# Kernel optimization log

Hardware: AMD Instinct MI355X
Metric: run time of the kernel (lower is better)

## Reference

```python
import jax, jax.numpy as jnp
import numpy as np

B, T, C = 128, 512, 128  # batch, seq_len, num_tags


def setup_inputs() -> dict:
    key = jax.random.key(0)
    k1, k2, k3 = jax.random.split(key, 3)
    labels = jax.random.randint(k1, (B, T), 0, C)
    y_true = jax.nn.one_hot(labels, C, dtype=jnp.float32)  # dense one-hot targets
    y_pred = jax.random.normal(k2, (B, T, C), dtype=jnp.float32)  # emission scores
    mask = jnp.ones((B, T), dtype=jnp.float32)
    # glorot_uniform for (C,C): limit = sqrt(6/(C+C))
    limit = np.sqrt(6.0 / (C + C)).astype(np.float32)
    trans = jax.random.uniform(k3, (C, C), dtype=jnp.float32, minval=-limit, maxval=limit)
    return {"y_true": y_true, "y_pred": y_pred, "mask": mask, "trans": trans}


def reference(y_true, y_pred, mask, trans):
    # Faithful translation of ConditionalRandomField.dense_loss (lr_multiplier=1).
    m = mask[..., None]                      # (B,T,1)
    y_true = y_true * m
    y_pred = y_pred * m
    # real path score
    emission = jnp.einsum('bnc,bnc->b', y_true, y_pred)
    transition = jnp.einsum('bni,ij,bnj->b', y_true[:, :-1], trans, y_true[:, 1:])
    real_path_score = emission + transition  # (B,)
    # forward algorithm: sequential logsumexp recurrence (K.rnn equivalent)
    init = y_pred[:, 0]                      # (B,C)
    xs = (jnp.swapaxes(y_pred[:, 1:], 0, 1),  # (T-1,B,C)
          jnp.swapaxes(mask[:, 1:], 0, 1))    # (T-1,B)

    def step(state, xm):
        x_t, m_t = xm
        # state: (B,C) alpha; trans: (C,C)
        new = jax.nn.logsumexp(state[:, :, None] + trans[None, :, :], axis=1) + x_t
        state = jnp.where(m_t[:, None] > 0, new, state)  # masked steps carry prev state
        return state, None

    last, _ = jax.lax.scan(step, init, xs)
    all_paths_score = jax.nn.logsumexp(last, axis=1)  # (B,)
    return all_paths_score - real_path_score          # (B,) per-sample CRF NLL
```

## Files before the change

### kernel.cpp

```cpp
#include <hip/hip_runtime.h>

#define BB 128
#define TT 512
#define CC 128

typedef short short8 __attribute__((ext_vector_type(8)));
typedef float f32x4  __attribute__((ext_vector_type(4)));
typedef unsigned u32x4 __attribute__((ext_vector_type(4)));
typedef unsigned u32x2 __attribute__((ext_vector_type(2)));

__device__ __forceinline__ unsigned pk_trunc(float a, float b) {
    return __builtin_amdgcn_perm(__float_as_uint(a), __float_as_uint(b), 0x03020706u);
}
__device__ __forceinline__ unsigned short f2bf(float f) {
    unsigned u = __float_as_uint(f);
    u += 0x7fffu + ((u >> 16) & 1u);
    return (unsigned short)(u >> 16);
}
__device__ __forceinline__ float lo16f(unsigned u) { return __uint_as_float(u << 16); }
__device__ __forceinline__ float hi16f(unsigned u) { return __uint_as_float(u & 0xffff0000u); }

#define MFMA16(A, B, C) __builtin_amdgcn_mfma_f32_16x16x32_bf16((A), (B), (C), 0, 0, 0)

__global__ __launch_bounds__(256, 1) void crf_all(
    const float* __restrict__ y_true, const float* __restrict__ y_pred,
    const float* __restrict__ mask, const float* __restrict__ trans,
    float* __restrict__ out)
{
    __shared__ __align__(16) unsigned sbuf[2][1024];
    __shared__ float red[4][16];

    const int tid  = threadIdx.x;
    const int lane = tid & 63;
    const int w    = tid >> 6;
    const int bq   = lane & 15;
    const int q    = lane >> 4;

    if (blockIdx.x >= 8) {
        const int rb  = blockIdx.x - 8;
        const int ts  = w * 128;
        const int te  = min(ts + 128, TT - 1);
        const float* yt_b = y_true + (size_t)rb * TT * CC;
        const float* yp_b = y_pred + (size_t)rb * TT * CC;
        const float* m_b  = mask + (size_t)rb * TT;

        float em = 0.f, tr = 0.f;
        int lprev = 0; float mprev = 0.f;
        const float* ytr = yt_b + ts * CC;
        const float* ypr = yp_b + ts * CC;
        float cyt0 = ytr[lane], cyt1 = ytr[lane + 64];
        float cyp0 = ypr[lane], cyp1 = ypr[lane + 64];
        float cm = m_b[ts];
        for (int t = ts; t <= te; ++t) {
            float nyt0 = 0.f, nyt1 = 0.f, nyp0 = 0.f, nyp1 = 0.f, nm = 0.f;
            if (t < te) {
                const float* ytn = yt_b + (t + 1) * CC;
                const float* ypn = yp_b + (t + 1) * CC;
                nyt0 = ytn[lane]; nyt1 = ytn[lane + 64];
                nyp0 = ypn[lane]; nyp1 = ypn[lane + 64];
                nm = m_b[t + 1];
            }
            unsigned long long b0 = __ballot(cyt0 > 0.5f);
            unsigned long long b1 = __ballot(cyt1 > 0.5f);
            int l = b0 ? (__ffsll(b0) - 1) : (64 + __ffsll(b1) - 1);
            float v0 = __shfl(cyp0, l & 63);
            float v1 = __shfl(cyp1, l & 63);
            float v  = (l < 64) ? v0 : v1;
            if (lane == 0) {
                if (t < ts + 128) em += cm * cm * v;
                if (t > ts)       tr += mprev * cm * trans[lprev * CC + l];
            }
            lprev = l; mprev = cm;
            cyt0 = nyt0; cyt1 = nyt1; cyp0 = nyp0; cyp1 = nyp1; cm = nm;
        }
        if (lane == 0) atomicAdd(&out[rb], -(em + tr));
        return;
    }

    const int g = blockIdx.x;
    const float* yb   = y_pred + (size_t)(g * 16 + bq) * TT * CC;
    const float* mrow = mask + (size_t)(g * 16 + bq) * TT;
    const int ch0 = 32 * w + 4 * q;

    const float4 i0 = *(const float4*)(yb + ch0);
    const float4 i1 = *(const float4*)(yb + ch0 + 16);
    const float  m0 = mrow[0];
    float4 pfa[4], pfb[4]; float pfm[4];
    #pragma unroll
    for (int p = 0; p < 4; ++p) {
        pfa[p] = *(const float4*)(yb + (size_t)(1 + p) * CC + ch0);
        pfb[p] = *(const float4*)(yb + (size_t)(1 + p) * CC + ch0 + 16);
        pfm[p] = mrow[1 + p];
    }

    short8 Af[2][4];
    #pragma unroll
    for (int n2 = 0; n2 < 2; ++n2) {
        const int j = (2 * w + n2) * 16 + bq;
        #pragma unroll
        for (int kt = 0; kt < 4; ++kt) {
            #pragma unroll
            for (int e = 0; e < 8; ++e)
                Af[n2][kt][e] = (short)f2bf(__expf(trans[(kt * 32 + q * 8 + e) * CC + j]));
        }
    }

    const int swz = (bq & 7) << 2;
    const int rw0 = bq * 64 + (( 0 + 4 * q) ^ swz);
    const int rw1 = bq * 64 + ((16 + 4 * q) ^ swz);
    const int rw2 = bq * 64 + ((32 + 4 * q) ^ swz);
    const int rw3 = bq * 64 + ((48 + 4 * q) ^ swz);
    const int ww0 = bq * 64 + ((16 * w + 2 * q) ^ swz);
    const int ww1 = bq * 64 + ((16 * w + 8 + 2 * q) ^ swz);

    {
        unsigned p0 = pk_trunc(__expf(i0.x * m0), __expf(i0.y * m0));
        unsigned p1 = pk_trunc(__expf(i0.z * m0), __expf(i0.w * m0));
        unsigned p2 = pk_trunc(__expf(i1.x * m0), __expf(i1.y * m0));
        unsigned p3 = pk_trunc(__expf(i1.z * m0), __expf(i1.w * m0));
        u32x2 a; a[0] = p0; a[1] = p1;
        u32x2 b; b[0] = p2; b[1] = p3;
        *(u32x2*)(&sbuf[0][0] + ww0) = a;
        *(u32x2*)(&sbuf[0][0] + ww1) = b;
    }
    asm volatile("s_waitcnt lgkmcnt(0)" ::: "memory");
    __builtin_amdgcn_s_barrier();
    asm volatile("" ::: "memory");

    float lacc = 0.f;

    auto dostep = [&](const int p, const int rpar, const bool ap, const int tn) {
        const unsigned* sb = &sbuf[rpar][0];
        unsigned* sw = &sbuf[rpar ^ 1][0];
        u32x4 B0 = *(const u32x4*)(sb + rw0);
        u32x4 B1 = *(const u32x4*)(sb + rw1);
        u32x4 B2 = *(const u32x4*)(sb + rw2);
        u32x4 B3 = *(const u32x4*)(sb + rw3);
        float pend = 1.f;
        if (ap) {
            float bc = __shfl(lo16f(B0[0]), bq, 64);
            pend = __builtin_amdgcn_rcpf(bc);
            lacc += __logf(bc);
        }
        union { u32x4 u; short8 s; } c0, c1, c2, c3;
        c0.u = B0; c1.u = B1; c2.u = B2; c3.u = B3;
        f32x4 a0 = {0.f, 0.f, 0.f, 0.f}, a1 = {0.f, 0.f, 0.f, 0.f};
        a0 = MFMA16(Af[0][0], c0.s, a0); a0 = MFMA16(Af[0][1], c1.s, a0);
        a0 = MFMA16(Af[0][2], c2.s, a0); a0 = MFMA16(Af[0][3], c3.s, a0);
        a1 = MFMA16(Af[1][0], c0.s, a1); a1 = MFMA16(Af[1][1], c1.s, a1);
        a1 = MFMA16(Af[1][2], c2.s, a1); a1 = MFMA16(Af[1][3], c3.s, a1);
        const float mm = pfm[p];
        const float4 va = pfa[p], vb = pfb[p];
        float e0 = __expf(va.x * mm), e1 = __expf(va.y * mm);
        float e2 = __expf(va.z * mm), e3 = __expf(va.w * mm);
        float f0 = __expf(vb.x * mm), f1 = __expf(vb.y * mm);
        float f2 = __expf(vb.z * mm), f3 = __expf(vb.w * mm);
        float v0 = a0[0] * e0, v1 = a0[1] * e1, v2 = a0[2] * e2, v3 = a0[3] * e3;
        float u0 = a1[0] * f0, u1 = a1[1] * f1, u2 = a1[2] * f2, u3 = a1[3] * f3;
        if (ap) {
            v0 *= pend; v1 *= pend; v2 *= pend; v3 *= pend;
            u0 *= pend; u1 *= pend; u2 *= pend; u3 *= pend;
        }
        unsigned n0 = pk_trunc(v0, v1), n1 = pk_trunc(v2, v3);
        unsigned n2 = pk_trunc(u0, u1), n3 = pk_trunc(u2, u3);
        if (__ballot(mm <= 0.f)) {
            u32x2 o0 = *(const u32x2*)(sb + ww0);
            u32x2 o1 = *(const u32x2*)(sb + ww1);
            unsigned k0 = pk_trunc(lo16f(o0[0]) * pend, hi16f(o0[0]) * pend);
            unsigned k1 = pk_trunc(lo16f(o0[1]) * pend, hi16f(o0[1]) * pend);
            unsigned k2 = pk_trunc(lo16f(o1[0]) * pend, hi16f(o1[0]) * pend);
            unsigned k3 = pk_trunc(lo16f(o1[1]) * pend, hi16f(o1[1]) * pend);
            const bool kk = (mm <= 0.f);
            n0 = kk ? k0 : n0; n1 = kk ? k1 : n1;
            n2 = kk ? k2 : n2; n3 = kk ? k3 : n3;
        }
        u32x2 wv0; wv0[0] = n0; wv0[1] = n1;
        u32x2 wv1; wv1[0] = n2; wv1[1] = n3;
        *(u32x2*)(sw + ww0) = wv0;
        *(u32x2*)(sw + ww1) = wv1;
        if (tn >= 0) {
            pfa[p] = *(const float4*)(yb + (size_t)tn * CC + ch0);
            pfb[p] = *(const float4*)(yb + (size_t)tn * CC + ch0 + 16);
            pfm[p] = mrow[tn];
        }
        asm volatile("s_waitcnt lgkmcnt(0)" ::: "memory");
        __builtin_amdgcn_s_barrier();
        asm volatile("" ::: "memory");
    };

    for (int tt = 1; tt <= 505; tt += 4) {
        int t4 = tt + 4, t5 = tt + 5, t6 = tt + 6, t7 = tt + 7;
        if (t7 > TT - 1) t7 = TT - 1;
        dostep(0, 0, true,  t4);
        dostep(1, 1, false, t5);
        dostep(2, 0, false, t6);
        dostep(3, 1, false, t7);
    }
    dostep(0, 0, true,  -1);
    dostep(1, 1, false, -1);

    {
        const unsigned* sb = &sbuf[0][0];
        u32x4 B0 = *(const u32x4*)(sb + rw0);
        u32x4 B1 = *(const u32x4*)(sb + rw1);
        u32x4 B2 = *(const u32x4*)(sb + rw2);
        u32x4 B3 = *(const u32x4*)(sb + rw3);
        union { u32x4 u; short8 s; } c0, c1, c2, c3;
        c0.u = B0; c1.u = B1; c2.u = B2; c3.u = B3;
        f32x4 a0 = {0.f, 0.f, 0.f, 0.f}, a1 = {0.f, 0.f, 0.f, 0.f};
        a0 = MFMA16(Af[0][0], c0.s, a0); a0 = MFMA16(Af[0][1], c1.s, a0);
        a0 = MFMA16(Af[0][2], c2.s, a0); a0 = MFMA16(Af[0][3], c3.s, a0);
        a1 = MFMA16(Af[1][0], c0.s, a1); a1 = MFMA16(Af[1][1], c1.s, a1);
        a1 = MFMA16(Af[1][2], c2.s, a1); a1 = MFMA16(Af[1][3], c3.s, a1);
        const float mm = pfm[2];
        const float4 va = pfa[2], vb = pfb[2];
        float e0 = __expf(va.x * mm), e1 = __expf(va.y * mm);
        float e2 = __expf(va.z * mm), e3 = __expf(va.w * mm);
        float f0 = __expf(vb.x * mm), f1 = __expf(vb.y * mm);
        float f2 = __expf(vb.z * mm), f3 = __expf(vb.w * mm);
        float ssum = a0[0] * e0 + a0[1] * e1 + a0[2] * e2 + a0[3] * e3
                   + a1[0] * f0 + a1[1] * f1 + a1[2] * f2 + a1[3] * f3;
        if (__ballot(mm <= 0.f)) {
            u32x2 o0 = *(const u32x2*)(sb + ww0);
            u32x2 o1 = *(const u32x2*)(sb + ww1);
            float os = lo16f(o0[0]) + hi16f(o0[0]) + lo16f(o0[1]) + hi16f(o0[1])
                     + lo16f(o1[0]) + hi16f(o1[0]) + lo16f(o1[1]) + hi16f(o1[1]);
            ssum = (mm <= 0.f) ? os : ssum;
        }
        ssum += __shfl_xor(ssum, 16, 64);
        ssum += __shfl_xor(ssum, 32, 64);
        if (lane < 16) red[w][lane] = ssum;
        asm volatile("s_waitcnt lgkmcnt(0)" ::: "memory");
        __builtin_amdgcn_s_barrier();
        asm volatile("" ::: "memory");
        if (w == 0 && lane < 16) {
            float tot = red[0][lane] + red[1][lane] + red[2][lane] + red[3][lane];
            atomicAdd(&out[g * 16 + lane], __logf(tot) + lacc);
        }
    }
}

extern "C" void kernel_launch(void* const* d_in, const int* in_sizes, int n_in,
                              void* d_out, int out_size, void* d_ws, size_t ws_size,
                              hipStream_t stream) {
    (void)in_sizes; (void)n_in; (void)out_size; (void)d_ws; (void)ws_size;
    const float* y_true = (const float*)d_in[0];
    const float* y_pred = (const float*)d_in[1];
    const float* mask   = (const float*)d_in[2];
    const float* trans  = (const float*)d_in[3];
    float* out = (float*)d_out;

    hipMemsetAsync(out, 0, BB * sizeof(float), stream);
    crf_all<<<dim3(8 + BB), 256, 0, stream>>>(y_true, y_pred, mask, trans, out);
}
```

Baseline: 255.7 us.

## Pack two batch groups per 512-thread block in forward recurrence

Doubles the block size to 512 threads so each forward-algorithm block handles two independent 16-sample groups, with separate LDS buffers and reductions per half. Grid shrinks from 8+128 to 4+128 blocks, and the real-path blocks split the sequence into 64-step chunks over 8 waves. The two groups now share every block-wide barrier, so each step's sync has to wait for both groups. The intent is better latency hiding from having more waves per CU on the serial recurrence.

```diff
diff --git a/kernel.cpp b/kernel.cpp
--- a/kernel.cpp
+++ b/kernel.cpp
@@ -22,13 +22,13 @@
 
 #define MFMA16(A, B, C) __builtin_amdgcn_mfma_f32_16x16x32_bf16((A), (B), (C), 0, 0, 0)
 
-__global__ __launch_bounds__(256, 1) void crf_all(
+__global__ __launch_bounds__(512, 1) void crf_all(
     const float* __restrict__ y_true, const float* __restrict__ y_pred,
     const float* __restrict__ mask, const float* __restrict__ trans,
     float* __restrict__ out)
 {
-    __shared__ __align__(16) unsigned sbuf[2][1024];
-    __shared__ float red[4][16];
+    __shared__ __align__(16) unsigned sbuf[2][2][1024];
+    __shared__ float red[2][4][16];
 
     const int tid  = threadIdx.x;
     const int lane = tid & 63;
@@ -36,10 +36,10 @@
     const int bq   = lane & 15;
     const int q    = lane >> 4;
 
-    if (blockIdx.x >= 8) {
-        const int rb  = blockIdx.x - 8;
-        const int ts  = w * 128;
-        const int te  = min(ts + 128, TT - 1);
+    if (blockIdx.x >= 4) {
+        const int rb  = blockIdx.x - 4;
+        const int ts  = w * 64;
+        const int te  = min(ts + 64, TT - 1);
         const float* yt_b = y_true + (size_t)rb * TT * CC;
         const float* yp_b = y_pred + (size_t)rb * TT * CC;
         const float* m_b  = mask + (size_t)rb * TT;
@@ -67,8 +67,8 @@
             float v1 = __shfl(cyp1, l & 63);
             float v  = (l < 64) ? v0 : v1;
             if (lane == 0) {
-                if (t < ts + 128) em += cm * cm * v;
-                if (t > ts)       tr += mprev * cm * trans[lprev * CC + l];
+                if (t < ts + 64) em += cm * cm * v;
+                if (t > ts)      tr += mprev * cm * trans[lprev * CC + l];
             }
             lprev = l; mprev = cm;
             cyt0 = nyt0; cyt1 = nyt1; cyp0 = nyp0; cyp1 = nyp1; cm = nm;
@@ -77,10 +77,12 @@
         return;
     }
 
-    const int g = blockIdx.x;
+    const int h  = w >> 2;
+    const int wv = w & 3;
+    const int g  = blockIdx.x * 2 + h;
     const float* yb   = y_pred + (size_t)(g * 16 + bq) * TT * CC;
     const float* mrow = mask + (size_t)(g * 16 + bq) * TT;
-    const int ch0 = 32 * w + 4 * q;
+    const int ch0 = 32 * wv + 4 * q;
 
     const float4 i0 = *(const float4*)(yb + ch0);
     const float4 i1 = *(const float4*)(yb + ch0 + 16);
@@ -96,7 +98,7 @@
     short8 Af[2][4];
     #pragma unroll
     for (int n2 = 0; n2 < 2; ++n2) {
-        const int j = (2 * w + n2) * 16 + bq;
+        const int j = (2 * wv + n2) * 16 + bq;
         #pragma unroll
         for (int kt = 0; kt < 4; ++kt) {
             #pragma unroll
@@ -110,8 +112,8 @@
     const int rw1 = bq * 64 + ((16 + 4 * q) ^ swz);
     const int rw2 = bq * 64 + ((32 + 4 * q) ^ swz);
     const int rw3 = bq * 64 + ((48 + 4 * q) ^ swz);
-    const int ww0 = bq * 64 + ((16 * w + 2 * q) ^ swz);
-    const int ww1 = bq * 64 + ((16 * w + 8 + 2 * q) ^ swz);
+    const int ww0 = bq * 64 + ((16 * wv + 2 * q) ^ swz);
+    const int ww1 = bq * 64 + ((16 * wv + 8 + 2 * q) ^ swz);
 
     {
         unsigned p0 = pk_trunc(__expf(i0.x * m0), __expf(i0.y * m0));
@@ -120,8 +122,8 @@
         unsigned p3 = pk_trunc(__expf(i1.z * m0), __expf(i1.w * m0));
         u32x2 a; a[0] = p0; a[1] = p1;
         u32x2 b; b[0] = p2; b[1] = p3;
-        *(u32x2*)(&sbuf[0][0] + ww0) = a;
-        *(u32x2*)(&sbuf[0][0] + ww1) = b;
+        *(u32x2*)(&sbuf[h][0][0] + ww0) = a;
+        *(u32x2*)(&sbuf[h][0][0] + ww1) = b;
     }
     asm volatile("s_waitcnt lgkmcnt(0)" ::: "memory");
     __builtin_amdgcn_s_barrier();
@@ -130,8 +132,8 @@
     float lacc = 0.f;
 
     auto dostep = [&](const int p, const int rpar, const bool ap, const int tn) {
-        const unsigned* sb = &sbuf[rpar][0];
-        unsigned* sw = &sbuf[rpar ^ 1][0];
+        const unsigned* sb = &sbuf[h][rpar][0];
+        unsigned* sw = &sbuf[h][rpar ^ 1][0];
         u32x4 B0 = *(const u32x4*)(sb + rw0);
         u32x4 B1 = *(const u32x4*)(sb + rw1);
         u32x4 B2 = *(const u32x4*)(sb + rw2);
@@ -200,7 +202,7 @@
     dostep(1, 1, false, -1);
 
     {
-        const unsigned* sb = &sbuf[0][0];
+        const unsigned* sb = &sbuf[h][0][0];
         u32x4 B0 = *(const u32x4*)(sb + rw0);
         u32x4 B1 = *(const u32x4*)(sb + rw1);
         u32x4 B2 = *(const u32x4*)(sb + rw2);
@@ -229,12 +231,13 @@
         }
         ssum += __shfl_xor(ssum, 16, 64);
         ssum += __shfl_xor(ssum, 32, 64);
-        if (lane < 16) red[w][lane] = ssum;
+        if (lane < 16) red[h][wv][lane] = ssum;
         asm volatile("s_waitcnt lgkmcnt(0)" ::: "memory");
         __builtin_amdgcn_s_barrier();
         asm volatile("" ::: "memory");
-        if (w == 0 && lane < 16) {
-            float tot = red[0][lane] + red[1][lane] + red[2][lane] + red[3][lane];
+        if (wv == 0 && lane < 16) {
+            float tot = red[h][0][lane] + red[h][1][lane]
+                      + red[h][2][lane] + red[h][3][lane];
             atomicAdd(&out[g * 16 + lane], __logf(tot) + lacc);
         }
     }
@@ -251,5 +254,5 @@
     float* out = (float*)d_out;
 
     hipMemsetAsync(out, 0, BB * sizeof(float), stream);
-    crf_all<<<dim3(8 + BB), 256, 0, stream>>>(y_true, y_pred, mask, trans, out);
-}
+    crf_all<<<dim3(4 + BB), 512, 0, stream>>>(y_true, y_pred, mask, trans, out);
+}
```

Result: slower. 419.2 us (+64.0%).

## Split scan and real-path into separate kernels, use two waves per scan block

Applied to the files above, without the earlier changes.

The forward-recurrence scan now runs in its own kernel with 128 threads (two waves) per block, each wave owning 64 output tags and issuing four MFMA tiles per k-step. This halves the number of waves taking part in each per-step barrier. The real-path score moves to a separate kernel launched afterwards on the same stream. The cost is twice the MFMA and exp work per wave, more registers, and an extra launch that may no longer overlap with the scan.

```diff
diff --git a/kernel.cpp b/kernel.cpp
--- a/kernel.cpp
+++ b/kernel.cpp
@@ -22,13 +22,12 @@
 
 #define MFMA16(A, B, C) __builtin_amdgcn_mfma_f32_16x16x32_bf16((A), (B), (C), 0, 0, 0)
 
-__global__ __launch_bounds__(256, 1) void crf_all(
-    const float* __restrict__ y_true, const float* __restrict__ y_pred,
-    const float* __restrict__ mask, const float* __restrict__ trans,
-    float* __restrict__ out)
+__global__ __launch_bounds__(128, 1) void crf_scan(
+    const float* __restrict__ y_pred, const float* __restrict__ mask,
+    const float* __restrict__ trans, float* __restrict__ out)
 {
     __shared__ __align__(16) unsigned sbuf[2][1024];
-    __shared__ float red[4][16];
+    __shared__ float red[2][16];
 
     const int tid  = threadIdx.x;
     const int lane = tid & 63;
@@ -36,72 +35,33 @@
     const int bq   = lane & 15;
     const int q    = lane >> 4;
 
-    if (blockIdx.x >= 8) {
-        const int rb  = blockIdx.x - 8;
-        const int ts  = w * 128;
-        const int te  = min(ts + 128, TT - 1);
-        const float* yt_b = y_true + (size_t)rb * TT * CC;
-        const float* yp_b = y_pred + (size_t)rb * TT * CC;
-        const float* m_b  = mask + (size_t)rb * TT;
-
-        float em = 0.f, tr = 0.f;
-        int lprev = 0; float mprev = 0.f;
-        const float* ytr = yt_b + ts * CC;
-        const float* ypr = yp_b + ts * CC;
-        float cyt0 = ytr[lane], cyt1 = ytr[lane + 64];
-        float cyp0 = ypr[lane], cyp1 = ypr[lane + 64];
-        float cm = m_b[ts];
-        for (int t = ts; t <= te; ++t) {
-            float nyt0 = 0.f, nyt1 = 0.f, nyp0 = 0.f, nyp1 = 0.f, nm = 0.f;
-            if (t < te) {
-                const float* ytn = yt_b + (t + 1) * CC;
-                const float* ypn = yp_b + (t + 1) * CC;
-                nyt0 = ytn[lane]; nyt1 = ytn[lane + 64];
-                nyp0 = ypn[lane]; nyp1 = ypn[lane + 64];
-                nm = m_b[t + 1];
-            }
-            unsigned long long b0 = __ballot(cyt0 > 0.5f);
-            unsigned long long b1 = __ballot(cyt1 > 0.5f);
-            int l = b0 ? (__ffsll(b0) - 1) : (64 + __ffsll(b1) - 1);
-            float v0 = __shfl(cyp0, l & 63);
-            float v1 = __shfl(cyp1, l & 63);
-            float v  = (l < 64) ? v0 : v1;
-            if (lane == 0) {
-                if (t < ts + 128) em += cm * cm * v;
-                if (t > ts)       tr += mprev * cm * trans[lprev * CC + l];
-            }
-            lprev = l; mprev = cm;
-            cyt0 = nyt0; cyt1 = nyt1; cyp0 = nyp0; cyp1 = nyp1; cm = nm;
-        }
-        if (lane == 0) atomicAdd(&out[rb], -(em + tr));
-        return;
-    }
-
     const int g = blockIdx.x;
     const float* yb   = y_pred + (size_t)(g * 16 + bq) * TT * CC;
     const float* mrow = mask + (size_t)(g * 16 + bq) * TT;
-    const int ch0 = 32 * w + 4 * q;
-
-    const float4 i0 = *(const float4*)(yb + ch0);
-    const float4 i1 = *(const float4*)(yb + ch0 + 16);
-    const float  m0 = mrow[0];
-    float4 pfa[4], pfb[4]; float pfm[4];
+    const int ch0 = 64 * w + 4 * q;
+
+    float4 i4[4];
+    #pragma unroll
+    for (int c = 0; c < 4; ++c) i4[c] = *(const float4*)(yb + ch0 + 16 * c);
+    const float m0 = mrow[0];
+    float4 pf[4][4]; float pfm[4];
     #pragma unroll
     for (int p = 0; p < 4; ++p) {
-        pfa[p] = *(const float4*)(yb + (size_t)(1 + p) * CC + ch0);
-        pfb[p] = *(const float4*)(yb + (size_t)(1 + p) * CC + ch0 + 16);
+        #pragma unroll
+        for (int c = 0; c < 4; ++c)
+            pf[p][c] = *(const float4*)(yb + (size_t)(1 + p) * CC + ch0 + 16 * c);
         pfm[p] = mrow[1 + p];
     }
 
-    short8 Af[2][4];
-    #pragma unroll
-    for (int n2 = 0; n2 < 2; ++n2) {
-        const int j = (2 * w + n2) * 16 + bq;
+    short8 Af[4][4];
+    #pragma unroll
+    for (int nt = 0; nt < 4; ++nt) {
+        const int j = (4 * w + nt) * 16 + bq;
         #pragma unroll
         for (int kt = 0; kt < 4; ++kt) {
             #pragma unroll
             for (int e = 0; e < 8; ++e)
-                Af[n2][kt][e] = (short)f2bf(__expf(trans[(kt * 32 + q * 8 + e) * CC + j]));
+                Af[nt][kt][e] = (short)f2bf(__expf(trans[(kt * 32 + q * 8 + e) * CC + j]));
         }
     }
 
@@ -110,18 +70,17 @@
     const int rw1 = bq * 64 + ((16 + 4 * q) ^ swz);
     const int rw2 = bq * 64 + ((32 + 4 * q) ^ swz);
     const int rw3 = bq * 64 + ((48 + 4 * q) ^ swz);
-    const int ww0 = bq * 64 + ((16 * w + 2 * q) ^ swz);
-    const int ww1 = bq * 64 + ((16 * w + 8 + 2 * q) ^ swz);
-
-    {
-        unsigned p0 = pk_trunc(__expf(i0.x * m0), __expf(i0.y * m0));
-        unsigned p1 = pk_trunc(__expf(i0.z * m0), __expf(i0.w * m0));
-        unsigned p2 = pk_trunc(__expf(i1.x * m0), __expf(i1.y * m0));
-        unsigned p3 = pk_trunc(__expf(i1.z * m0), __expf(i1.w * m0));
+    int ww[4];
+    #pragma unroll
+    for (int nt = 0; nt < 4; ++nt)
+        ww[nt] = bq * 64 + ((32 * w + 8 * nt + 2 * q) ^ swz);
+
+    #pragma unroll
+    for (int c = 0; c < 4; ++c) {
+        unsigned p0 = pk_trunc(__expf(i4[c].x * m0), __expf(i4[c].y * m0));
+        unsigned p1 = pk_trunc(__expf(i4[c].z * m0), __expf(i4[c].w * m0));
         u32x2 a; a[0] = p0; a[1] = p1;
-        u32x2 b; b[0] = p2; b[1] = p3;
-        *(u32x2*)(&sbuf[0][0] + ww0) = a;
-        *(u32x2*)(&sbuf[0][0] + ww1) = b;
+        *(u32x2*)(&sbuf[0][0] + ww[c]) = a;
     }
     asm volatile("s_waitcnt lgkmcnt(0)" ::: "memory");
     __builtin_amdgcn_s_barrier();
@@ -136,6 +95,13 @@
         u32x4 B1 = *(const u32x4*)(sb + rw1);
         u32x4 B2 = *(const u32x4*)(sb + rw2);
         u32x4 B3 = *(const u32x4*)(sb + rw3);
+        const float mm = pfm[p];
+        float e[4][4];
+        #pragma unroll
+        for (int c = 0; c < 4; ++c) {
+            e[c][0] = __expf(pf[p][c].x * mm); e[c][1] = __expf(pf[p][c].y * mm);
+            e[c][2] = __expf(pf[p][c].z * mm); e[c][3] = __expf(pf[p][c].w * mm);
+        }
         float pend = 1.f;
         if (ap) {
             float bc = __shfl(lo16f(B0[0]), bq, 64);
@@ -144,43 +110,46 @@
         }
         union { u32x4 u; short8 s; } c0, c1, c2, c3;
         c0.u = B0; c1.u = B1; c2.u = B2; c3.u = B3;
-        f32x4 a0 = {0.f, 0.f, 0.f, 0.f}, a1 = {0.f, 0.f, 0.f, 0.f};
-        a0 = MFMA16(Af[0][0], c0.s, a0); a0 = MFMA16(Af[0][1], c1.s, a0);
-        a0 = MFMA16(Af[0][2], c2.s, a0); a0 = MFMA16(Af[0][3], c3.s, a0);
-        a1 = MFMA16(Af[1][0], c0.s, a1); a1 = MFMA16(Af[1][1], c1.s, a1);
-        a1 = MFMA16(Af[1][2], c2.s, a1); a1 = MFMA16(Af[1][3], c3.s, a1);
-        const float mm = pfm[p];
-        const float4 va = pfa[p], vb = pfb[p];
-        float e0 = __expf(va.x * mm), e1 = __expf(va.y * mm);
-        float e2 = __expf(va.z * mm), e3 = __expf(va.w * mm);
-        float f0 = __expf(vb.x * mm), f1 = __expf(vb.y * mm);
-        float f2 = __expf(vb.z * mm), f3 = __expf(vb.w * mm);
-        float v0 = a0[0] * e0, v1 = a0[1] * e1, v2 = a0[2] * e2, v3 = a0[3] * e3;
-        float u0 = a1[0] * f0, u1 = a1[1] * f1, u2 = a1[2] * f2, u3 = a1[3] * f3;
-        if (ap) {
-            v0 *= pend; v1 *= pend; v2 *= pend; v3 *= pend;
-            u0 *= pend; u1 *= pend; u2 *= pend; u3 *= pend;
-        }
-        unsigned n0 = pk_trunc(v0, v1), n1 = pk_trunc(v2, v3);
-        unsigned n2 = pk_trunc(u0, u1), n3 = pk_trunc(u2, u3);
+        f32x4 acc[4];
+        #pragma unroll
+        for (int nt = 0; nt < 4; ++nt) { f32x4 z = {0.f,0.f,0.f,0.f}; acc[nt] = z; }
+        #pragma unroll
+        for (int nt = 0; nt < 4; ++nt) acc[nt] = MFMA16(Af[nt][0], c0.s, acc[nt]);
+        #pragma unroll
+        for (int nt = 0; nt < 4; ++nt) acc[nt] = MFMA16(Af[nt][1], c1.s, acc[nt]);
+        #pragma unroll
+        for (int nt = 0; nt < 4; ++nt) acc[nt] = MFMA16(Af[nt][2], c2.s, acc[nt]);
+        #pragma unroll
+        for (int nt = 0; nt < 4; ++nt) acc[nt] = MFMA16(Af[nt][3], c3.s, acc[nt]);
+        unsigned nn[4][2];
+        #pragma unroll
+        for (int nt = 0; nt < 4; ++nt) {
+            float v0 = acc[nt][0] * e[nt][0], v1 = acc[nt][1] * e[nt][1];
+            float v2 = acc[nt][2] * e[nt][2], v3 = acc[nt][3] * e[nt][3];
+            if (ap) { v0 *= pend; v1 *= pend; v2 *= pend; v3 *= pend; }
+            nn[nt][0] = pk_trunc(v0, v1);
+            nn[nt][1] = pk_trunc(v2, v3);
+        }
         if (__ballot(mm <= 0.f)) {
-            u32x2 o0 = *(const u32x2*)(sb + ww0);
-            u32x2 o1 = *(const u32x2*)(sb + ww1);
-            unsigned k0 = pk_trunc(lo16f(o0[0]) * pend, hi16f(o0[0]) * pend);
-            unsigned k1 = pk_trunc(lo16f(o0[1]) * pend, hi16f(o0[1]) * pend);
-            unsigned k2 = pk_trunc(lo16f(o1[0]) * pend, hi16f(o1[0]) * pend);
-            unsigned k3 = pk_trunc(lo16f(o1[1]) * pend, hi16f(o1[1]) * pend);
-            const bool kk = (mm <= 0.f);
-            n0 = kk ? k0 : n0; n1 = kk ? k1 : n1;
-            n2 = kk ? k2 : n2; n3 = kk ? k3 : n3;
-        }
-        u32x2 wv0; wv0[0] = n0; wv0[1] = n1;
-        u32x2 wv1; wv1[0] = n2; wv1[1] = n3;
-        *(u32x2*)(sw + ww0) = wv0;
-        *(u32x2*)(sw + ww1) = wv1;
+            #pragma unroll
+            for (int nt = 0; nt < 4; ++nt) {
+                u32x2 o = *(const u32x2*)(sb + ww[nt]);
+                unsigned k0 = pk_trunc(lo16f(o[0]) * pend, hi16f(o[0]) * pend);
+                unsigned k1 = pk_trunc(lo16f(o[1]) * pend, hi16f(o[1]) * pend);
+                const bool kk = (mm <= 0.f);
+                nn[nt][0] = kk ? k0 : nn[nt][0];
+                nn[nt][1] = kk ? k1 : nn[nt][1];
+            }
+        }
+        #pragma unroll
+        for (int nt = 0; nt < 4; ++nt) {
+            u32x2 wv2; wv2[0] = nn[nt][0]; wv2[1] = nn[nt][1];
+            *(u32x2*)(sw + ww[nt]) = wv2;
+        }
         if (tn >= 0) {
-            pfa[p] = *(const float4*)(yb + (size_t)tn * CC + ch0);
-            pfb[p] = *(const float4*)(yb + (size_t)tn * CC + ch0 + 16);
+            #pragma unroll
+            for (int c = 0; c < 4; ++c)
+                pf[p][c] = *(const float4*)(yb + (size_t)tn * CC + ch0 + 16 * c);
             pfm[p] = mrow[tn];
         }
         asm volatile("s_waitcnt lgkmcnt(0)" ::: "memory");
@@ -205,26 +174,38 @@
         u32x4 B1 = *(const u32x4*)(sb + rw1);
         u32x4 B2 = *(const u32x4*)(sb + rw2);
         u32x4 B3 = *(const u32x4*)(sb + rw3);
+        const float mm = pfm[2];
+        float e[4][4];
+        #pragma unroll
+        for (int c = 0; c < 4; ++c) {
+            e[c][0] = __expf(pf[2][c].x * mm); e[c][1] = __expf(pf[2][c].y * mm);
+            e[c][2] = __expf(pf[2][c].z * mm); e[c][3] = __expf(pf[2][c].w * mm);
+        }
         union { u32x4 u; short8 s; } c0, c1, c2, c3;
         c0.u = B0; c1.u = B1; c2.u = B2; c3.u = B3;
-        f32x4 a0 = {0.f, 0.f, 0.f, 0.f}, a1 = {0.f, 0.f, 0.f, 0.f};
-        a0 = MFMA16(Af[0][0], c0.s, a0); a0 = MFMA16(Af[0][1], c1.s, a0);
-        a0 = MFMA16(Af[0][2], c2.s, a0); a0 = MFMA16(Af[0][3], c3.s, a0);
-        a1 = MFMA16(Af[1][0], c0.s, a1); a1 = MFMA16(Af[1][1], c1.s, a1);
-        a1 = MFMA16(Af[1][2], c2.s, a1); a1 = MFMA16(Af[1][3], c3.s, a1);
-        const float mm = pfm[2];
-        const float4 va = pfa[2], vb = pfb[2];
-        float e0 = __expf(va.x * mm), e1 = __expf(va.y * mm);
-        float e2 = __expf(va.z * mm), e3 = __expf(va.w * mm);
-        float f0 = __expf(vb.x * mm), f1 = __expf(vb.y * mm);
-        float f2 = __expf(vb.z * mm), f3 = __expf(vb.w * mm);
-        float ssum = a0[0] * e0 + a0[1] * e1 + a0[2] * e2 + a0[3] * e3
-                   + a1[0] * f0 + a1[1] * f1 + a1[2] * f2 + a1[3] * f3;
+        f32x4 acc[4];
+        #pragma unroll
+        for (int nt = 0; nt < 4; ++nt) { f32x4 z = {0.f,0.f,0.f,0.f}; acc[nt] = z; }
+        #pragma unroll
+        for (int nt = 0; nt < 4; ++nt) acc[nt] = MFMA16(Af[nt][0], c0.s, acc[nt]);
+        #pragma unroll
+        for (int nt = 0; nt < 4; ++nt) acc[nt] = MFMA16(Af[nt][1], c1.s, acc[nt]);
+        #pragma unroll
+        for (int nt = 0; nt < 4; ++nt) acc[nt] = MFMA16(Af[nt][2], c2.s, acc[nt]);
+        #pragma unroll
+        for (int nt = 0; nt < 4; ++nt) acc[nt] = MFMA16(Af[nt][3], c3.s, acc[nt]);
+        float ssum = 0.f;
+        #pragma unroll
+        for (int nt = 0; nt < 4; ++nt)
+            ssum += acc[nt][0] * e[nt][0] + acc[nt][1] * e[nt][1]
+                  + acc[nt][2] * e[nt][2] + acc[nt][3] * e[nt][3];
         if (__ballot(mm <= 0.f)) {
-            u32x2 o0 = *(const u32x2*)(sb + ww0);
-            u32x2 o1 = *(const u32x2*)(sb + ww1);
-            float os = lo16f(o0[0]) + hi16f(o0[0]) + lo16f(o0[1]) + hi16f(o0[1])
-                     + lo16f(o1[0]) + hi16f(o1[0]) + lo16f(o1[1]) + hi16f(o1[1]);
+            float os = 0.f;
+            #pragma unroll
+            for (int nt = 0; nt < 4; ++nt) {
+                u32x2 o = *(const u32x2*)(sb + ww[nt]);
+                os += lo16f(o[0]) + hi16f(o[0]) + lo16f(o[1]) + hi16f(o[1]);
+            }
             ssum = (mm <= 0.f) ? os : ssum;
         }
         ssum += __shfl_xor(ssum, 16, 64);
@@ -234,10 +215,57 @@
         __builtin_amdgcn_s_barrier();
         asm volatile("" ::: "memory");
         if (w == 0 && lane < 16) {
-            float tot = red[0][lane] + red[1][lane] + red[2][lane] + red[3][lane];
+            float tot = red[0][lane] + red[1][lane];
             atomicAdd(&out[g * 16 + lane], __logf(tot) + lacc);
         }
     }
+}
+
+__global__ __launch_bounds__(256, 1) void crf_real(
+    const float* __restrict__ y_true, const float* __restrict__ y_pred,
+    const float* __restrict__ mask, const float* __restrict__ trans,
+    float* __restrict__ out)
+{
+    const int tid  = threadIdx.x;
+    const int lane = tid & 63;
+    const int w    = tid >> 6;
+    const int rb   = blockIdx.x;
+    const int ts   = w * 128;
+    const int te   = min(ts + 128, TT - 1);
+    const float* yt_b = y_true + (size_t)rb * TT * CC;
+    const float* yp_b = y_pred + (size_t)rb * TT * CC;
+    const float* m_b  = mask + (size_t)rb * TT;
+
+    float em = 0.f, tr = 0.f;
+    int lprev = 0; float mprev = 0.f;
+    const float* ytr = yt_b + ts * CC;
+    const float* ypr = yp_b + ts * CC;
+    float cyt0 = ytr[lane], cyt1 = ytr[lane + 64];
+    float cyp0 = ypr[lane], cyp1 = ypr[lane + 64];
+    float cm = m_b[ts];
+    for (int t = ts; t <= te; ++t) {
+        float nyt0 = 0.f, nyt1 = 0.f, nyp0 = 0.f, nyp1 = 0.f, nm = 0.f;
+        if (t < te) {
+            const float* ytn = yt_b + (t + 1) * CC;
+            const float* ypn = yp_b + (t + 1) * CC;
+            nyt0 = ytn[lane]; nyt1 = ytn[lane + 64];
+            nyp0 = ypn[lane]; nyp1 = ypn[lane + 64];
+            nm = m_b[t + 1];
+        }
+        unsigned long long b0 = __ballot(cyt0 > 0.5f);
+        unsigned long long b1 = __ballot(cyt1 > 0.5f);
+        int l = b0 ? (__ffsll(b0) - 1) : (64 + __ffsll(b1) - 1);
+        float v0 = __shfl(cyp0, l & 63);
+        float v1 = __shfl(cyp1, l & 63);
+        float v  = (l < 64) ? v0 : v1;
+        if (lane == 0) {
+            if (t < ts + 128) em += cm * cm * v;
+            if (t > ts)       tr += mprev * cm * trans[lprev * CC + l];
+        }
+        lprev = l; mprev = cm;
+        cyt0 = nyt0; cyt1 = nyt1; cyp0 = nyp0; cyp1 = nyp1; cm = nm;
+    }
+    if (lane == 0) atomicAdd(&out[rb], -(em + tr));
 }
 
 extern "C" void kernel_launch(void* const* d_in, const int* in_sizes, int n_in,
@@ -251,5 +279,6 @@
     float* out = (float*)d_out;
 
     hipMemsetAsync(out, 0, BB * sizeof(float), stream);
-    crf_all<<<dim3(8 + BB), 256, 0, stream>>>(y_true, y_pred, mask, trans, out);
-}
+    crf_scan<<<dim3(8), 128, 0, stream>>>(y_pred, mask, trans, out);
+    crf_real<<<dim3(BB), 256, 0, stream>>>(y_true, y_pred, mask, trans, out);
+}
```

Result: slower. 352.2 us (+37.7%).

## Keep own-wave state slice in registers via shuffles, reorder K-tiles per wave

Applied to the files above, without the earlier changes.

Each wave now builds the MFMA B-operand for its own 32-channel K-slice directly from the values it just produced, using cross-lane shuffles, instead of reading them back from LDS. It rotates the K-tile order per wave so the register-held slice goes first and can issue before the LDS reads of the other three slices land. The MFMA chain is split into two independent accumulators to shorten the dependency chain, and the normaliser is read straight from LDS instead of through a shuffle. This aims to cut LDS read latency and serial MFMA dependency in the per-timestep critical path, at the cost of extra shuffle instructions and registers.

```diff
diff --git a/kernel.cpp b/kernel.cpp
--- a/kernel.cpp
+++ b/kernel.cpp
@@ -21,6 +21,86 @@
 __device__ __forceinline__ float hi16f(unsigned u) { return __uint_as_float(u & 0xffff0000u); }
 
 #define MFMA16(A, B, C) __builtin_amdgcn_mfma_f32_16x16x32_bf16((A), (B), (C), 0, 0, 0)
+
+#define BUILD_BFO(n00, n01, n10, n11) do {                                     \
+    const int sA_ = bq + 16 * ((2 * q) & 3);                                   \
+    const int sB_ = bq + 16 * ((2 * q + 1) & 3);                               \
+    unsigned a00 = __shfl((n00), sA_, 64), a10 = __shfl((n10), sA_, 64);       \
+    unsigned a01 = __shfl((n01), sA_, 64), a11 = __shfl((n11), sA_, 64);       \
+    unsigned b00 = __shfl((n00), sB_, 64), b10 = __shfl((n10), sB_, 64);       \
+    unsigned b01 = __shfl((n01), sB_, 64), b11 = __shfl((n11), sB_, 64);       \
+    const bool hi_ = (q >> 1) != 0;                                            \
+    BfO[0] = hi_ ? a10 : a00;                                                  \
+    BfO[1] = hi_ ? a11 : a01;                                                  \
+    BfO[2] = hi_ ? b10 : b00;                                                  \
+    BfO[3] = hi_ ? b11 : b01;                                                  \
+} while (0)
+
+#define DOSTEP(AP_, P_, RPAR_, TN_) do {                                       \
+    const unsigned* sb = &sbuf[RPAR_][0];                                      \
+    unsigned* sw = &sbuf[(RPAR_) ^ 1][0];                                      \
+    u32x4 Rv1 = *(const u32x4*)(sb + rd1);                                     \
+    u32x4 Rv2 = *(const u32x4*)(sb + rd2);                                     \
+    u32x4 Rv3 = *(const u32x4*)(sb + rd3);                                     \
+    unsigned bcu = 0;                                                          \
+    if (AP_) bcu = sb[bcaddr];                    \
+    const float mm = pfm[P_];                                                  \
+    float e0[4], e1[4];                                                        \
+    e0[0] = __expf(pfa[P_].x * mm); e0[1] = __expf(pfa[P_].y * mm);            \
+    e0[2] = __expf(pfa[P_].z * mm); e0[3] = __expf(pfa[P_].w * mm);            \
+    e1[0] = __expf(pfb[P_].x * mm); e1[1] = __expf(pfb[P_].y * mm);            \
+    e1[2] = __expf(pfb[P_].z * mm); e1[3] = __expf(pfb[P_].w * mm);            \
+    union { u32x4 u; short8 s; } cO, c1, c2, c3;                               \
+    cO.u[0] = BfO[0]; cO.u[1] = BfO[1]; cO.u[2] = BfO[2]; cO.u[3] = BfO[3];    \
+    c1.u = Rv1; c2.u = Rv2; c3.u = Rv3;                                        \
+    f32x4 aA0 = {0.f,0.f,0.f,0.f}, aA1 = {0.f,0.f,0.f,0.f};                    \
+    f32x4 aB0 = {0.f,0.f,0.f,0.f}, aB1 = {0.f,0.f,0.f,0.f};                    \
+    aA0 = MFMA16(AfP[0][0], cO.s, aA0);  aA1 = MFMA16(AfP[1][0], cO.s, aA1);   \
+    aA0 = MFMA16(AfP[0][1], c1.s, aA0);  aA1 = MFMA16(AfP[1][1], c1.s, aA1);   \
+    aB0 = MFMA16(AfP[0][2], c2.s, aB0);  aB1 = MFMA16(AfP[1][2], c2.s, aB1);   \
+    aB0 = MFMA16(AfP[0][3], c3.s, aB0);  aB1 = MFMA16(AfP[1][3], c3.s, aB1);   \
+    f32x4 ac0 = aA0 + aB0, ac1 = aA1 + aB1;                                    \
+    float pend = 1.f;                                                          \
+    if (AP_) {                                                                 \
+        float bc = lo16f(bcu);                                                 \
+        pend = __builtin_amdgcn_rcpf(bc);                                      \
+        lacc += __logf(bc);                                                    \
+    }                                                                          \
+    float v00 = ac0[0]*e0[0], v01 = ac0[1]*e0[1];                              \
+    float v02 = ac0[2]*e0[2], v03 = ac0[3]*e0[3];                              \
+    float v10 = ac1[0]*e1[0], v11 = ac1[1]*e1[1];                              \
+    float v12 = ac1[2]*e1[2], v13 = ac1[3]*e1[3];                              \
+    if (AP_) {                                                                 \
+        v00 *= pend; v01 *= pend; v02 *= pend; v03 *= pend;                    \
+        v10 *= pend; v11 *= pend; v12 *= pend; v13 *= pend;                    \
+    }                                                                          \
+    unsigned n00 = pk_trunc(v00, v01), n01 = pk_trunc(v02, v03);               \
+    unsigned n10 = pk_trunc(v10, v11), n11 = pk_trunc(v12, v13);               \
+    if (__ballot(mm <= 0.f)) {                  \
+        u32x2 o0 = *(const u32x2*)(sb + wwA);                                  \
+        u32x2 o1 = *(const u32x2*)(sb + wwB);                                  \
+        unsigned k00 = pk_trunc(lo16f(o0[0]) * pend, hi16f(o0[0]) * pend);     \
+        unsigned k01 = pk_trunc(lo16f(o0[1]) * pend, hi16f(o0[1]) * pend);     \
+        unsigned k10 = pk_trunc(lo16f(o1[0]) * pend, hi16f(o1[0]) * pend);     \
+        unsigned k11 = pk_trunc(lo16f(o1[1]) * pend, hi16f(o1[1]) * pend);     \
+        const bool kk = (mm <= 0.f);                                           \
+        n00 = kk ? k00 : n00; n01 = kk ? k01 : n01;                            \
+        n10 = kk ? k10 : n10; n11 = kk ? k11 : n11;                            \
+    }                                                                          \
+    u32x2 wv0; wv0[0] = n00; wv0[1] = n01;                                     \
+    u32x2 wv1; wv1[0] = n10; wv1[1] = n11;                                     \
+    *(u32x2*)(sw + wwA) = wv0;                                                 \
+    *(u32x2*)(sw + wwB) = wv1;                                                 \
+    BUILD_BFO(n00, n01, n10, n11);                \
+    if ((TN_) >= 0) {                                  \
+        pfa[P_] = *(const float4*)(yb + (size_t)(TN_) * CC + ch0);             \
+        pfb[P_] = *(const float4*)(yb + (size_t)(TN_) * CC + ch0 + 16);        \
+        pfm[P_] = mrow[TN_];                                                   \
+    }                                                                          \
+    asm volatile("s_waitcnt lgkmcnt(0)" ::: "memory");                         \
+    __builtin_amdgcn_s_barrier();                 \
+    asm volatile("" ::: "memory");                                             \
+} while (0)
 
 __global__ __launch_bounds__(256, 1) void crf_all(
     const float* __restrict__ y_true, const float* __restrict__ y_pred,
@@ -33,8 +113,6 @@
     const int tid  = threadIdx.x;
     const int lane = tid & 63;
     const int w    = tid >> 6;
-    const int bq   = lane & 15;
-    const int q    = lane >> 4;
 
     if (blockIdx.x >= 8) {
         const int rb  = blockIdx.x - 8;
@@ -77,7 +155,9 @@
         return;
     }
 
-    const int g = blockIdx.x;
+    const int bq = lane & 15;
+    const int q  = lane >> 4;
+    const int g  = blockIdx.x;
     const float* yb   = y_pred + (size_t)(g * 16 + bq) * TT * CC;
     const float* mrow = mask + (size_t)(g * 16 + bq) * TT;
     const int ch0 = 32 * w + 4 * q;
@@ -93,35 +173,39 @@
         pfm[p] = mrow[1 + p];
     }
 
-    short8 Af[2][4];
+    short8 AfP[2][4];
     #pragma unroll
     for (int n2 = 0; n2 < 2; ++n2) {
         const int j = (2 * w + n2) * 16 + bq;
         #pragma unroll
-        for (int kt = 0; kt < 4; ++kt) {
+        for (int i = 0; i < 4; ++i) {
+            const int kt = (w + i) & 3;
             #pragma unroll
             for (int e = 0; e < 8; ++e)
-                Af[n2][kt][e] = (short)f2bf(__expf(trans[(kt * 32 + q * 8 + e) * CC + j]));
+                AfP[n2][i][e] = (short)f2bf(__expf(trans[(kt * 32 + q * 8 + e) * CC + j]));
         }
     }
 
     const int swz = (bq & 7) << 2;
-    const int rw0 = bq * 64 + (( 0 + 4 * q) ^ swz);
-    const int rw1 = bq * 64 + ((16 + 4 * q) ^ swz);
-    const int rw2 = bq * 64 + ((32 + 4 * q) ^ swz);
-    const int rw3 = bq * 64 + ((48 + 4 * q) ^ swz);
-    const int ww0 = bq * 64 + ((16 * w + 2 * q) ^ swz);
-    const int ww1 = bq * 64 + ((16 * w + 8 + 2 * q) ^ swz);
+    const int rd1 = bq * 64 + ((((w + 1) & 3) * 16 + 4 * q) ^ swz);
+    const int rd2 = bq * 64 + ((((w + 2) & 3) * 16 + 4 * q) ^ swz);
+    const int rd3 = bq * 64 + ((((w + 3) & 3) * 16 + 4 * q) ^ swz);
+    const int wwA = bq * 64 + ((16 * w + 2 * q) ^ swz);
+    const int wwB = bq * 64 + ((16 * w + 8 + 2 * q) ^ swz);
+    const int bcaddr = bq * 64 + swz;
+
+    unsigned BfO[4];
 
     {
-        unsigned p0 = pk_trunc(__expf(i0.x * m0), __expf(i0.y * m0));
-        unsigned p1 = pk_trunc(__expf(i0.z * m0), __expf(i0.w * m0));
-        unsigned p2 = pk_trunc(__expf(i1.x * m0), __expf(i1.y * m0));
-        unsigned p3 = pk_trunc(__expf(i1.z * m0), __expf(i1.w * m0));
-        u32x2 a; a[0] = p0; a[1] = p1;
-        u32x2 b; b[0] = p2; b[1] = p3;
-        *(u32x2*)(&sbuf[0][0] + ww0) = a;
-        *(u32x2*)(&sbuf[0][0] + ww1) = b;
+        unsigned n00 = pk_trunc(__expf(i0.x * m0), __expf(i0.y * m0));
+        unsigned n01 = pk_trunc(__expf(i0.z * m0), __expf(i0.w * m0));
+        unsigned n10 = pk_trunc(__expf(i1.x * m0), __expf(i1.y * m0));
+        unsigned n11 = pk_trunc(__expf(i1.z * m0), __expf(i1.w * m0));
+        u32x2 a; a[0] = n00; a[1] = n01;
+        u32x2 b; b[0] = n10; b[1] = n11;
+        *(u32x2*)(&sbuf[0][0] + wwA) = a;
+        *(u32x2*)(&sbuf[0][0] + wwB) = b;
+        BUILD_BFO(n00, n01, n10, n11);
     }
     asm volatile("s_waitcnt lgkmcnt(0)" ::: "memory");
     __builtin_amdgcn_s_barrier();
@@ -129,100 +213,43 @@
 
     float lacc = 0.f;
 
-    auto dostep = [&](const int p, const int rpar, const bool ap, const int tn) {
-        const unsigned* sb = &sbuf[rpar][0];
-        unsigned* sw = &sbuf[rpar ^ 1][0];
-        u32x4 B0 = *(const u32x4*)(sb + rw0);
-        u32x4 B1 = *(const u32x4*)(sb + rw1);
-        u32x4 B2 = *(const u32x4*)(sb + rw2);
-        u32x4 B3 = *(const u32x4*)(sb + rw3);
-        float pend = 1.f;
-        if (ap) {
-            float bc = __shfl(lo16f(B0[0]), bq, 64);
-            pend = __builtin_amdgcn_rcpf(bc);
-            lacc += __logf(bc);
-        }
-        union { u32x4 u; short8 s; } c0, c1, c2, c3;
-        c0.u = B0; c1.u = B1; c2.u = B2; c3.u = B3;
-        f32x4 a0 = {0.f, 0.f, 0.f, 0.f}, a1 = {0.f, 0.f, 0.f, 0.f};
-        a0 = MFMA16(Af[0][0], c0.s, a0); a0 = MFMA16(Af[0][1], c1.s, a0);
-        a0 = MFMA16(Af[0][2], c2.s, a0); a0 = MFMA16(Af[0][3], c3.s, a0);
-        a1 = MFMA16(Af[1][0], c0.s, a1); a1 = MFMA16(Af[1][1], c1.s, a1);
-        a1 = MFMA16(Af[1][2], c2.s, a1); a1 = MFMA16(Af[1][3], c3.s, a1);
-        const float mm = pfm[p];
-        const float4 va = pfa[p], vb = pfb[p];
-        float e0 = __expf(va.x * mm), e1 = __expf(va.y * mm);
-        float e2 = __expf(va.z * mm), e3 = __expf(va.w * mm);
-        float f0 = __expf(vb.x * mm), f1 = __expf(vb.y * mm);
-        float f2 = __expf(vb.z * mm), f3 = __expf(vb.w * mm);
-        float v0 = a0[0] * e0, v1 = a0[1] * e1, v2 = a0[2] * e2, v3 = a0[3] * e3;
-        float u0 = a1[0] * f0, u1 = a1[1] * f1, u2 = a1[2] * f2, u3 = a1[3] * f3;
-        if (ap) {
-            v0 *= pend; v1 *= pend; v2 *= pend; v3 *= pend;
-            u0 *= pend; u1 *= pend; u2 *= pend; u3 *= pend;
-        }
-        unsigned n0 = pk_trunc(v0, v1), n1 = pk_trunc(v2, v3);
-        unsigned n2 = pk_trunc(u0, u1), n3 = pk_trunc(u2, u3);
-        if (__ballot(mm <= 0.f)) {
-            u32x2 o0 = *(const u32x2*)(sb + ww0);
-            u32x2 o1 = *(const u32x2*)(sb + ww1);
-            unsigned k0 = pk_trunc(lo16f(o0[0]) * pend, hi16f(o0[0]) * pend);
-            unsigned k1 = pk_trunc(lo16f(o0[1]) * pend, hi16f(o0[1]) * pend);
-            unsigned k2 = pk_trunc(lo16f(o1[0]) * pend, hi16f(o1[0]) * pend);
-            unsigned k3 = pk_trunc(lo16f(o1[1]) * pend, hi16f(o1[1]) * pend);
-            const bool kk = (mm <= 0.f);
-            n0 = kk ? k0 : n0; n1 = kk ? k1 : n1;
-            n2 = kk ? k2 : n2; n3 = kk ? k3 : n3;
-        }
-        u32x2 wv0; wv0[0] = n0; wv0[1] = n1;
-        u32x2 wv1; wv1[0] = n2; wv1[1] = n3;
-        *(u32x2*)(sw + ww0) = wv0;
-        *(u32x2*)(sw + ww1) = wv1;
-        if (tn >= 0) {
-            pfa[p] = *(const float4*)(yb + (size_t)tn * CC + ch0);
-            pfb[p] = *(const float4*)(yb + (size_t)tn * CC + ch0 + 16);
-            pfm[p] = mrow[tn];
-        }
-        asm volatile("s_waitcnt lgkmcnt(0)" ::: "memory");
-        __builtin_amdgcn_s_barrier();
-        asm volatile("" ::: "memory");
-    };
-
     for (int tt = 1; tt <= 505; tt += 4) {
         int t4 = tt + 4, t5 = tt + 5, t6 = tt + 6, t7 = tt + 7;
         if (t7 > TT - 1) t7 = TT - 1;
-        dostep(0, 0, true,  t4);
-        dostep(1, 1, false, t5);
-        dostep(2, 0, false, t6);
-        dostep(3, 1, false, t7);
-    }
-    dostep(0, 0, true,  -1);
-    dostep(1, 1, false, -1);
+        DOSTEP(true,  0, 0, t4);
+        DOSTEP(false, 1, 1, t5);
+        DOSTEP(false, 2, 0, t6);
+        DOSTEP(false, 3, 1, t7);
+    }
+    DOSTEP(true,  0, 0, -1);
+    DOSTEP(false, 1, 1, -1);
 
     {
         const unsigned* sb = &sbuf[0][0];
-        u32x4 B0 = *(const u32x4*)(sb + rw0);
-        u32x4 B1 = *(const u32x4*)(sb + rw1);
-        u32x4 B2 = *(const u32x4*)(sb + rw2);
-        u32x4 B3 = *(const u32x4*)(sb + rw3);
-        union { u32x4 u; short8 s; } c0, c1, c2, c3;
-        c0.u = B0; c1.u = B1; c2.u = B2; c3.u = B3;
-        f32x4 a0 = {0.f, 0.f, 0.f, 0.f}, a1 = {0.f, 0.f, 0.f, 0.f};
-        a0 = MFMA16(Af[0][0], c0.s, a0); a0 = MFMA16(Af[0][1], c1.s, a0);
-        a0 = MFMA16(Af[0][2], c2.s, a0); a0 = MFMA16(Af[0][3], c3.s, a0);
-        a1 = MFMA16(Af[1][0], c0.s, a1); a1 = MFMA16(Af[1][1], c1.s, a1);
-        a1 = MFMA16(Af[1][2], c2.s, a1); a1 = MFMA16(Af[1][3], c3.s, a1);
+        u32x4 Rv1 = *(const u32x4*)(sb + rd1);
+        u32x4 Rv2 = *(const u32x4*)(sb + rd2);
+        u32x4 Rv3 = *(const u32x4*)(sb + rd3);
         const float mm = pfm[2];
-        const float4 va = pfa[2], vb = pfb[2];
-        float e0 = __expf(va.x * mm), e1 = __expf(va.y * mm);
-        float e2 = __expf(va.z * mm), e3 = __expf(va.w * mm);
-        float f0 = __expf(vb.x * mm), f1 = __expf(vb.y * mm);
-        float f2 = __expf(vb.z * mm), f3 = __expf(vb.w * mm);
-        float ssum = a0[0] * e0 + a0[1] * e1 + a0[2] * e2 + a0[3] * e3
-                   + a1[0] * f0 + a1[1] * f1 + a1[2] * f2 + a1[3] * f3;
+        float e0[4], e1[4];
+        e0[0] = __expf(pfa[2].x * mm); e0[1] = __expf(pfa[2].y * mm);
+        e0[2] = __expf(pfa[2].z * mm); e0[3] = __expf(pfa[2].w * mm);
+        e1[0] = __expf(pfb[2].x * mm); e1[1] = __expf(pfb[2].y * mm);
+        e1[2] = __expf(pfb[2].z * mm); e1[3] = __expf(pfb[2].w * mm);
+        union { u32x4 u; short8 s; } cO, c1, c2, c3;
+        cO.u[0] = BfO[0]; cO.u[1] = BfO[1]; cO.u[2] = BfO[2]; cO.u[3] = BfO[3];
+        c1.u = Rv1; c2.u = Rv2; c3.u = Rv3;
+        f32x4 aA0 = {0.f,0.f,0.f,0.f}, aA1 = {0.f,0.f,0.f,0.f};
+        f32x4 aB0 = {0.f,0.f,0.f,0.f}, aB1 = {0.f,0.f,0.f,0.f};
+        aA0 = MFMA16(AfP[0][0], cO.s, aA0);  aA1 = MFMA16(AfP[1][0], cO.s, aA1);
+        aA0 = MFMA16(AfP[0][1], c1.s, aA0);  aA1 = MFMA16(AfP[1][1], c1.s, aA1);
+        aB0 = MFMA16(AfP[0][2], c2.s, aB0);  aB1 = MFMA16(AfP[1][2], c2.s, aB1);
+        aB0 = MFMA16(AfP[0][3], c3.s, aB0);  aB1 = MFMA16(AfP[1][3], c3.s, aB1);
+        f32x4 ac0 = aA0 + aB0, ac1 = aA1 + aB1;
+        float ssum = ac0[0]*e0[0] + ac0[1]*e0[1] + ac0[2]*e0[2] + ac0[3]*e0[3]
+                   + ac1[0]*e1[0] + ac1[1]*e1[1] + ac1[2]*e1[2] + ac1[3]*e1[3];
         if (__ballot(mm <= 0.f)) {
-            u32x2 o0 = *(const u32x2*)(sb + ww0);
-            u32x2 o1 = *(const u32x2*)(sb + ww1);
+            u32x2 o0 = *(const u32x2*)(sb + wwA);
+            u32x2 o1 = *(const u32x2*)(sb + wwB);
             float os = lo16f(o0[0]) + hi16f(o0[0]) + lo16f(o0[1]) + hi16f(o0[1])
                      + lo16f(o1[0]) + hi16f(o1[0]) + lo16f(o1[1]) + hi16f(o1[1]);
             ssum = (mm <= 0.f) ? os : ssum;
```

After: 274.4 us. +7.3%, slower.
